# Optimization experiments

Measured on AMD Instinct MI355X. Metric: run time of the kernel, lower is better.

## Reference

```python
import jax, jax.numpy as jnp
import numpy as np
import jax.scipy.signal as jss

SX, SY, C, K = 256, 256, 3, 10
C0 = [0, 0, 0, 1, 1, 1, 2, 2, 2, 0]
C1 = [[0, 1, 2, 9], [3, 4, 5], [6, 7, 8]]
DD, DT, SIGMA = 5, 0.2, 0.65

_KX = jnp.array([[-1., 0., 1.], [-2., 0., 2.], [-1., 0., 1.]])
_KY = _KX.T


def _conv2(A, Kf):
    # zero-padded 'same' 2D true convolution, vmapped over channel axis
    return jax.vmap(lambda a: jss.convolve2d(a, Kf, mode='same'), in_axes=2, out_axes=2)(A)


def sobel(A):
    # (X, Y, c) -> (X, Y, 2, c): [sobel_y, sobel_x] stacked on axis 2 (FlowLenia convention)
    return jnp.concatenate([_conv2(A, _KY)[:, :, None, :], _conv2(A, _KX)[:, :, None, :]], axis=2)


def growth(U, m, s):
    # bell(U,m,s)*2 - 1
    return jnp.exp(-((U - m) / s) ** 2 / 2.) * 2. - 1.


def get_kernels_fft(R, r, a, w, b):
    # FlowLenia kernel construction: ring distance -> smooth cutoff * sum-of-bumps, normalized, fft2(fftshift)
    mid = SX // 2
    xs = jnp.arange(-mid, mid, dtype=jnp.float32)
    D = jnp.sqrt(xs[:, None] ** 2 + xs[None, :] ** 2)            # (X, Y)
    Dk = D[..., None] / ((R + 15.) * r)                          # (X, Y, k)
    ker = (b * jnp.exp(-(Dk[..., None] - a) ** 2 / w)).sum(-1)   # (X, Y, k)
    sig = 0.5 * (jnp.tanh(-(Dk - 1.) * 10. / 2.) + 1.)           # sigmoid(-(D-1)*10)
    Kk = sig * ker
    nK = Kk / Kk.sum(axis=(0, 1), keepdims=True)
    return jnp.fft.fft2(jnp.fft.fftshift(nK, axes=(0, 1)), axes=(0, 1))


def _rt_apply(A, F):
    # Reintegration tracking with 'wall' border: flow-driven mass redistribution over a (2dd+1)^2 neighborhood
    ii = jnp.arange(SX, dtype=jnp.float32)
    pos = jnp.stack(jnp.meshgrid(ii, ii, indexing='ij'), axis=-1) + 0.5   # (X, Y, 2) cell centers
    ma = DD - SIGMA                                   # max flow magnitude
    mu = pos[..., None] + jnp.clip(DT * F, -ma, ma)   # (X, Y, 2, C) target centers
    mu = jnp.clip(mu, SIGMA, SX - SIGMA)              # wall border
    offs = jnp.arange(-DD, DD + 1)
    gx, gy = jnp.meshgrid(offs, offs, indexing='ij')
    dxs, dys = gx.reshape(-1), gy.reshape(-1)
    clip_hi = min(1., 2. * SIGMA)

    def step(dx, dy):
        Ar = jnp.roll(A, (dx, dy), axis=(0, 1))
        mur = jnp.roll(mu, (dx, dy), axis=(0, 1))
        dpmu = jnp.abs(pos[..., None] - mur)                                  # (X, Y, 2, C)
        sz = 0.5 - dpmu + SIGMA
        area = jnp.prod(jnp.clip(sz, 0., clip_hi), axis=2) / (4. * SIGMA ** 2)  # (X, Y, C)
        return Ar * area

    return jax.vmap(step)(dxs, dys).sum(axis=0)


def setup_inputs() -> dict:
    key = jax.random.key(0)
    ks = jax.random.split(key, 9)
    A = jax.random.uniform(ks[0], (SX, SY, C), dtype=jnp.float32)
    R = jax.random.uniform(ks[1], (), minval=2.0, maxval=25.0)
    r = jax.random.uniform(ks[2], (K,), minval=0.2, maxval=1.0)
    m = jax.random.uniform(ks[3], (K,), minval=0.05, maxval=0.5)
    s = jax.random.uniform(ks[4], (K,), minval=0.001, maxval=0.18)
    h = jax.random.uniform(ks[5], (K,), minval=0.01, maxval=1.0)
    a = jax.random.uniform(ks[6], (K, 3), minval=0.0, maxval=1.0)
    b = jax.random.uniform(ks[7], (K, 3), minval=0.001, maxval=1.0)
    w = jax.random.uniform(ks[8], (K, 3), minval=0.01, maxval=0.5)
    return dict(A=A, R=R, r=r, m=m, s=s, h=h, a=a, b=b, w=w)


def reference(A, R, r, m, s, h, a, b, w):
    fK = get_kernels_fft(R, r, a, w, b)                       # (X, Y, k) complex
    fA = jnp.fft.fft2(A, axes=(0, 1))
    fAk = fA[:, :, jnp.array(C0)]                             # (X, Y, k)
    U = jnp.real(jnp.fft.ifft2(fK * fAk, axes=(0, 1)))        # (X, Y, k)
    U = growth(U, m, s) * h
    U = jnp.dstack([U[:, :, C1[c]].sum(axis=-1) for c in range(C)])  # (X, Y, C)
    nabla_U = sobel(U)                                        # (X, Y, 2, C)
    nabla_A = sobel(A.sum(axis=-1, keepdims=True))            # (X, Y, 2, 1)
    alpha = jnp.clip((A[:, :, None, :] / C) ** 2, 0., 1.)     # (X, Y, 1, C)
    F = nabla_U * (1. - alpha) - nabla_A * alpha              # (X, Y, 2, C)
    return _rt_apply(A, F)
```

## Files before the change

kernel.cpp:

```cpp
#include <hip/hip_runtime.h>

#define NPIX 65536

#define OX1ARE(c) ((0  + (c))*NPIX)
#define OX1AIM(c) ((3  + (c))*NPIX)
#define OX1K(k)   ((6  + (k))*NPIX)
#define OX2ARE(c) ((16 + (c))*NPIX)
#define OX2AIM(c) ((19 + (c))*NPIX)
#define OX2K(k)   ((22 + (k))*NPIX)
#define OX3RE(j)  ((32 + (j))*NPIX)
#define OX3IM(j)  ((37 + (j))*NPIX)
#define OU(k)     ((42 + (k))*NPIX)
#define OPACK(c)  ((52 + 4*(c))*NPIX)
#define OROWS     (64*NPIX)

__device__ __forceinline__ void fft256_core(float* __restrict__ re, float* __restrict__ im,
                                            const float* __restrict__ twr,
                                            const float* __restrict__ twi, int lane) {
    #pragma unroll
    for (int s = 1; s <= 8; ++s) {
        int h = 1 << (s - 1);
        #pragma unroll
        for (int b = 0; b < 2; ++b) {
            int idx = b*64 + lane;
            int pos = idx & (h - 1);
            int g   = idx >> (s - 1);
            int i0 = (g << s) + pos;
            int i1 = i0 + h;
            int tj = pos << (8 - s);
            float wr = twr[tj], wi = twi[tj];
            float xr = re[i1], xi = im[i1];
            float br = fmaf(xr, wr, -xi*wi);
            float bi = fmaf(xr, wi,  xi*wr);
            float ar = re[i0], ai = im[i0];
            re[i0] = ar + br; im[i0] = ai + bi;
            re[i1] = ar - br; im[i1] = ai - bi;
        }
    }
}

__device__ __forceinline__ void build_tw(float* twr, float* twi, int t, float sgn) {
    if (t < 128) {
        float ang = (float)t * 0.0245436930f;
        twr[t] = cosf(ang);
        twi[t] = sgn * sinf(ang);
    }
}

__device__ __forceinline__ void store_t4(float* __restrict__ dst, const float* __restrict__ buf,
                                         int off, int t, int lb) {
    float4 v;
    v.x = buf[0*512 + off + t];
    v.y = buf[1*512 + off + t];
    v.z = buf[2*512 + off + t];
    v.w = buf[3*512 + off + t];
    *(float4*)&dst[t*256 + lb] = v;
}

struct KP { float rden, a0,a1,a2, b0,b1,b2, iw0,iw1,iw2; };

__device__ __forceinline__ void load_kp(KP& kp, int k, float R,
        const float* __restrict__ r_, const float* __restrict__ a_,
        const float* __restrict__ b_, const float* __restrict__ w_) {
    kp.rden = 1.0f / ((R + 15.0f) * r_[k]);
    kp.a0 = a_[k*3+0]; kp.a1 = a_[k*3+1]; kp.a2 = a_[k*3+2];
    kp.b0 = b_[k*3+0]; kp.b1 = b_[k*3+1]; kp.b2 = b_[k*3+2];
    kp.iw0 = 1.0f/w_[k*3+0]; kp.iw1 = 1.0f/w_[k*3+1]; kp.iw2 = 1.0f/w_[k*3+2];
}

__device__ __forceinline__ float kval(int di, int dj, const KP& kp) {
    float D  = sqrtf((float)(di*di + dj*dj));
    float Dk = D * kp.rden;
    if (Dk > 3.0f) return 0.0f;
    float d0 = Dk - kp.a0, d1 = Dk - kp.a1, d2 = Dk - kp.a2;
    float ker = kp.b0*expf(-(d0*d0)*kp.iw0)
              + kp.b1*expf(-(d1*d1)*kp.iw1)
              + kp.b2*expf(-(d2*d2)*kp.iw2);
    float sig = 1.0f / (1.0f + expf(10.0f*(Dk - 1.0f)));
    return sig * ker;
}

__global__ __launch_bounds__(256) void fwd_rows(const float* __restrict__ A,
        const float* __restrict__ R_, const float* __restrict__ r_,
        const float* __restrict__ a_, const float* __restrict__ b_,
        const float* __restrict__ w_, float* __restrict__ ws) {
    __shared__ float buf[4*512];
    __shared__ float twr[128], twi[128];
    int p  = blockIdx.x >> 6;
    int lb = (blockIdx.x & 63) * 4;
    int wid = threadIdx.x >> 6, lane = threadIdx.x & 63;
    int t = threadIdx.x;
    build_tw(twr, twi, t, -1.0f);
    int iw = lb + wid;
    float* re = &buf[wid*512];
    float* im = re + 256;

    int fa, fb;
    switch (p) {
        case 0:  fa = 0;  fb = 1;  break;
        case 1:  fa = 2;  fb = 12; break;
        case 2:  fa = 3;  fb = 4;  break;
        case 3:  fa = 5;  fb = 6;  break;
        case 4:  fa = 7;  fb = 8;  break;
        case 5:  fa = 9;  fb = 10; break;
        default: fa = 11; fb = -1; break;
    }
    bool aA = (fa < 3);
    bool bA = (fb >= 0 && fb < 3);
    float R = R_[0];
    int di = ((iw + 128) & 255) - 128;
    KP kpa, kpb;
    if (!aA)      load_kp(kpa, fa - 3, R, r_, a_, b_, w_);
    if (fb >= 3)  load_kp(kpb, fb - 3, R, r_, a_, b_, w_);
    float sum_a = 0.0f, sum_b = 0.0f;
    #pragma unroll
    for (int e = 0; e < 4; ++e) {
        int idx = e*64 + lane;
        int dst = __brev(idx) >> 24;
        int dj  = ((idx + 128) & 255) - 128;
        float vf, vg;
        if (aA) vf = A[(iw*256 + idx)*3 + fa];
        else    { vf = kval(di, dj, kpa); sum_a += vf; }
        if (fb < 0)      vg = 0.0f;
        else if (bA)     vg = A[(iw*256 + idx)*3 + fb];
        else             { vg = kval(di, dj, kpb); sum_b += vg; }
        re[dst] = vf;
        im[dst] = vg;
    }
    if (!aA) {
        float s = sum_a;
        #pragma unroll
        for (int off = 32; off; off >>= 1) s += __shfl_xor(s, off);
        if (lane == 0) ws[OROWS + (fa - 3)*256 + iw] = s;
    }
    if (fb >= 3) {
        float s = sum_b;
        #pragma unroll
        for (int off = 32; off; off >>= 1) s += __shfl_xor(s, off);
        if (lane == 0) ws[OROWS + (fb - 3)*256 + iw] = s;
    }
    __syncthreads();
    fft256_core(re, im, twr, twi, lane);
    __syncthreads();
    if (t <= 128) {
        if (p <= 1) {
            int u2 = (256 - t) & 255;
            float4 Fre, Fim, Gre, Gim;
            float* pF[4] = {&Fre.x, &Fim.x, &Gre.x, &Gim.x};
            #pragma unroll
            for (int l = 0; l < 4; ++l) {
                float zr1 = buf[l*512 + t],  zi1 = buf[l*512 + 256 + t];
                float zr2 = buf[l*512 + u2], zi2 = buf[l*512 + 256 + u2];
                pF[0][l] = 0.5f*(zr1 + zr2);
                pF[1][l] = 0.5f*(zi1 - zi2);
                pF[2][l] = 0.5f*(zi1 + zi2);
                pF[3][l] = 0.5f*(zr2 - zr1);
            }
            if (p == 0) {
                *(float4*)&ws[OX1ARE(0) + t*256 + lb] = Fre;
                *(float4*)&ws[OX1AIM(0) + t*256 + lb] = Fim;
                *(float4*)&ws[OX1ARE(1) + t*256 + lb] = Gre;
                *(float4*)&ws[OX1AIM(1) + t*256 + lb] = Gim;
            } else {
                *(float4*)&ws[OX1ARE(2) + t*256 + lb] = Fre;
                *(float4*)&ws[OX1AIM(2) + t*256 + lb] = Fim;
                *(float4*)&ws[OX1K(9)   + t*256 + lb] = Gre;
            }
        } else {
            float4 va, vb;
            float* pV[2] = {&va.x, &vb.x};
            #pragma unroll
            for (int l = 0; l < 4; ++l) {
                pV[0][l] = buf[l*512 + t];
                pV[1][l] = buf[l*512 + 256 + t];
            }
            *(float4*)&ws[OX1K(fa - 3) + t*256 + lb] = va;
            if (fb >= 0) *(float4*)&ws[OX1K(fb - 3) + t*256 + lb] = vb;
        }
    }
}

__global__ __launch_bounds__(256) void fwd_cols(float* __restrict__ ws) {
    __shared__ float buf[4*512];
    __shared__ float twr[128], twi[128];
    int bid = blockIdx.x;
    int wid = threadIdx.x >> 6, lane = threadIdx.x & 63;
    int t = threadIdx.x;
    build_tw(twr, twi, t, -1.0f);
    float* re = &buf[wid*512];
    float* im = re + 256;
    if (bid < 99) {
        int c  = bid / 33;
        int ub = (bid % 33) * 4;
        int u  = ub + wid; if (u > 128) u = 128;
        const float* rr = ws + OX1ARE(c) + u*256;
        const float* ri = ws + OX1AIM(c) + u*256;
        #pragma unroll
        for (int e = 0; e < 4; ++e) {
            int idx = e*64 + lane;
            int dst = __brev(idx) >> 24;
            re[dst] = rr[idx];
            im[dst] = ri[idx];
        }
        __syncthreads();
        fft256_core(re, im, twr, twi, lane);
        __syncthreads();
        store_t4(ws + OX2ARE(c), buf, 0,   t, ub);
        store_t4(ws + OX2AIM(c), buf, 256, t, ub);
    } else {
        int q  = (bid - 99) / 33;
        int ub = ((bid - 99) % 33) * 4;
        int u  = ub + wid; if (u > 128) u = 128;
        const float* ra = ws + OX1K(2*q)     + u*256;
        const float* rb = ws + OX1K(2*q + 1) + u*256;
        #pragma unroll
        for (int e = 0; e < 4; ++e) {
            int idx = e*64 + lane;
            int dst = __brev(idx) >> 24;
            re[dst] = ra[idx];
            im[dst] = rb[idx];
        }
        __syncthreads();
        fft256_core(re, im, twr, twi, lane);
        __syncthreads();
        if (t <= 128) {
            store_t4(ws + OX2K(2*q),     buf, 0,   t, ub);
            store_t4(ws + OX2K(2*q + 1), buf, 256, t, ub);
        }
    }
}

__global__ __launch_bounds__(256) void inv_rows(float* __restrict__ ws) {
    __shared__ float buf[4*512];
    __shared__ float twr[128], twi[128];
    int j  = blockIdx.x >> 6;
    int lb = (blockIdx.x & 63) * 4;
    int wid = threadIdx.x >> 6, lane = threadIdx.x & 63;
    int t = threadIdx.x;
    build_tw(twr, twi, t, 1.0f);
    int ka = 2*j, kb = 2*j + 1;
    int ca = (ka < 9) ? ka/3 : 0;
    int cb = (kb < 9) ? kb/3 : 0;
    int v  = lb + wid;
    int vr = (256 - v) & 255;
    int vf = (v <= 128) ? v : 256 - v;
    const float* Aare_v = ws + OX2ARE(ca) + v*256;
    const float* Aaim_v = ws + OX2AIM(ca) + v*256;
    const float* Aare_r = ws + OX2ARE(ca) + vr*256;
    const float* Aaim_r = ws + OX2AIM(ca) + vr*256;
    const float* Bare_v = ws + OX2ARE(cb) + v*256;
    const float* Baim_v = ws + OX2AIM(cb) + v*256;
    const float* Bare_r = ws + OX2ARE(cb) + vr*256;
    const float* Baim_r = ws + OX2AIM(cb) + vr*256;
    const float* Ka = ws + OX2K(ka) + vf*256;
    const float* Kb = ws + OX2K(kb) + vf*256;
    float* re = &buf[wid*512];
    float* im = re + 256;
    #pragma unroll
    for (int e = 0; e < 4; ++e) {
        int idx = e*64 + lane;
        int dst = __brev(idx) >> 24;
        bool hi = idx > 128;
        int uf = hi ? 256 - idx : idx;
        const float* pAr = hi ? Aare_r : Aare_v;
        const float* pAi = hi ? Aaim_r : Aaim_v;
        const float* pBr = hi ? Bare_r : Bare_v;
        const float* pBi = hi ? Baim_r : Baim_v;
        float ar = pAr[uf];
        float ai = pAi[uf]; ai = hi ? -ai : ai;
        float br = pBr[uf];
        float bi = pBi[uf]; bi = hi ? -bi : bi;
        float kva = Ka[uf], kvb = Kb[uf];
        float uar = ar*kva, uai = ai*kva;
        float ubr = br*kvb, ubi = bi*kvb;
        re[dst] = uar - ubi;
        im[dst] = uai + ubr;
    }
    __syncthreads();
    fft256_core(re, im, twr, twi, lane);
    __syncthreads();
    store_t4(ws + OX3RE(j), buf, 0,   t, lb);
    store_t4(ws + OX3IM(j), buf, 256, t, lb);
}

__global__ __launch_bounds__(256) void inv_cols(float* __restrict__ ws) {
    __shared__ float buf[4*512];
    __shared__ float twr[128], twi[128];
    int j  = blockIdx.x >> 6;
    int lb = (blockIdx.x & 63) * 4;
    int wid = threadIdx.x >> 6, lane = threadIdx.x & 63;
    int t = threadIdx.x;
    build_tw(twr, twi, t, 1.0f);
    float* re = &buf[wid*512];
    float* im = re + 256;
    const float* rr = ws + OX3RE(j) + (lb + wid)*256;
    const float* ri = ws + OX3IM(j) + (lb + wid)*256;
    #pragma unroll
    for (int e = 0; e < 4; ++e) {
        int idx = e*64 + lane;
        int dst = __brev(idx) >> 24;
        re[dst] = rr[idx];
        im[dst] = ri[idx];
    }
    __syncthreads();
    fft256_core(re, im, twr, twi, lane);
    __syncthreads();
    const float sc = 1.0f / 65536.0f;
    float4 va, vb;
    va.x = buf[0*512 + t] * sc;       vb.x = buf[0*512 + 256 + t] * sc;
    va.y = buf[1*512 + t] * sc;       vb.y = buf[1*512 + 256 + t] * sc;
    va.z = buf[2*512 + t] * sc;       vb.z = buf[2*512 + 256 + t] * sc;
    va.w = buf[3*512 + t] * sc;       vb.w = buf[3*512 + 256 + t] * sc;
    *(float4*)&ws[OU(2*j)     + t*256 + lb] = va;
    *(float4*)&ws[OU(2*j + 1) + t*256 + lb] = vb;
}

__global__ __launch_bounds__(256) void growth_mu(const float* __restrict__ A,
                                                 float* __restrict__ ws,
                                                 const float* __restrict__ m_,
                                                 const float* __restrict__ s_,
                                                 const float* __restrict__ h_) {
    __shared__ float Ush[3][256];
    __shared__ float As[3][256];
    __shared__ float kinv[4];
    int b = blockIdx.x;
    int c = b >> 8;
    int x = b & 255;
    int t = threadIdx.x, wid = t >> 6, lane = t & 63;
    int nk = (c == 0) ? 4 : 3;
    if (wid < nk) {
        int k = (wid == 3) ? 9 : c*3 + wid;
        const float* rw = ws + OROWS + k*256;
        float v = rw[lane] + rw[64+lane] + rw[128+lane] + rw[192+lane];
        #pragma unroll
        for (int off = 32; off; off >>= 1) v += __shfl_xor(v, off);
        if (lane == 0) kinv[wid] = 1.0f / v;
    }
    #pragma unroll
    for (int rr = 0; rr < 3; ++rr) {
        int xr = x - 1 + rr;
        float sv = 0.0f;
        if (xr >= 0 && xr <= 255) {
            int base = (xr*256 + t)*3;
            sv = A[base] + A[base + 1] + A[base + 2];
        }
        As[rr][t] = sv;
    }
    __syncthreads();
    for (int rr = 0; rr < 3; ++rr) {
        int xr = x - 1 + rr;
        float outv = 0.0f;
        if (xr >= 0 && xr <= 255) {
            int idx = xr*256 + t;
            for (int kk = 0; kk < nk; ++kk) {
                int k = (kk == 3) ? 9 : c*3 + kk;
                float U = ws[OU(k) + idx] * kinv[kk];
                float z = (U - m_[k]) / s_[k];
                outv += h_[k] * (expf(-0.5f*z*z)*2.0f - 1.0f);
            }
        }
        Ush[rr][t] = outv;
    }
    __syncthreads();
    int y = t;
    float vA[3][3], vU[3][3];
    #pragma unroll
    for (int ii = 0; ii < 3; ++ii)
        #pragma unroll
        for (int jj = 0; jj < 3; ++jj) {
            int yy = y - 1 + jj;
            bool ok = (yy >= 0 && yy <= 255);
            vA[ii][jj] = ok ? As[ii][yy]  : 0.0f;
            vU[ii][jj] = ok ? Ush[ii][yy] : 0.0f;
        }
    float gyA = (vA[0][0] + 2.0f*vA[0][1] + vA[0][2]) - (vA[2][0] + 2.0f*vA[2][1] + vA[2][2]);
    float gxA = (vA[0][0] + 2.0f*vA[1][0] + vA[2][0]) - (vA[0][2] + 2.0f*vA[1][2] + vA[2][2]);
    float gy  = (vU[0][0] + 2.0f*vU[0][1] + vU[0][2]) - (vU[2][0] + 2.0f*vU[2][1] + vU[2][2]);
    float gx  = (vU[0][0] + 2.0f*vU[1][0] + vU[2][0]) - (vU[0][2] + 2.0f*vU[1][2] + vU[2][2]);
    float a = A[(x*256 + y)*3 + c];
    float al = (a / 3.0f); al = al * al;
    al = fminf(fmaxf(al, 0.0f), 1.0f);
    float F0 = gy * (1.0f - al) - gyA * al;
    float F1 = gx * (1.0f - al) - gxA * al;
    float d0 = fminf(fmaxf(0.2f * F0, -4.35f), 4.35f);
    float d1 = fminf(fmaxf(0.2f * F1, -4.35f), 4.35f);
    float mux = fminf(fmaxf((float)x + 0.5f + d0, 0.65f), 255.35f);
    float muy = fminf(fmaxf((float)y + 0.5f + d1, 0.65f), 255.35f);
    float4 pk;
    pk.x = a;
    pk.y = mux - ((float)x + 0.5f);
    pk.z = muy;
    pk.w = 0.0f;
    *(float4*)&ws[OPACK(c) + (x*256 + y)*4] = pk;
}

__global__ __launch_bounds__(256) void rt_apply_v3(const float* __restrict__ ws,
                                                   float* __restrict__ out) {
    __shared__ float4 sP[11*256];
    int b = blockIdx.x;
    int c = b >> 8;
    int x = b & 255;
    const float4* pp = (const float4*)&ws[OPACK(c)];
    int t = threadIdx.x;
    #pragma unroll
    for (int i = 0; i < 11; ++i) {
        int xs = (x - (i - 5)) & 255;
        sP[i*256 + t] = pp[xs*256 + t];
    }
    __syncthreads();
    int y = t;
    float py = (float)y + 0.5f;
    float acc = 0.0f;
    #pragma unroll
    for (int i = 0; i < 11; ++i) {
        int xs = (x - (i - 5)) & 255;
        float dxf = (float)(x - xs);
        int rb = i * 256;
        #pragma unroll
        for (int dy = -5; dy <= 5; ++dy) {
            int sy = (y - dy) & 255;
            float4 v = sP[rb + sy];
            float ax = __builtin_amdgcn_fmed3f(1.15f - fabsf(dxf - v.y), 0.0f, 1.0f);
            float ay = __builtin_amdgcn_fmed3f(1.15f - fabsf(py  - v.z), 0.0f, 1.0f);
            acc = fmaf(v.x, ax * ay, acc);
        }
    }
    out[(x*256 + y)*3 + c] = acc * (1.0f / (4.0f * 0.65f * 0.65f));
}

extern "C" void kernel_launch(void* const* d_in, const int* in_sizes, int n_in,
                              void* d_out, int out_size, void* d_ws, size_t ws_size,
                              hipStream_t stream) {
    const float* A = (const float*)d_in[0];
    const float* R = (const float*)d_in[1];
    const float* r = (const float*)d_in[2];
    const float* m = (const float*)d_in[3];
    const float* s = (const float*)d_in[4];
    const float* h = (const float*)d_in[5];
    const float* a = (const float*)d_in[6];
    const float* b = (const float*)d_in[7];
    const float* w = (const float*)d_in[8];
    float* ws  = (float*)d_ws;
    float* out = (float*)d_out;

    fwd_rows<<<7*64, 256, 0, stream>>>(A, R, r, a, b, w, ws);
    fwd_cols<<<99 + 165, 256, 0, stream>>>(ws);
    inv_rows<<<5*64, 256, 0, stream>>>(ws);
    inv_cols<<<5*64, 256, 0, stream>>>(ws);
    growth_mu<<<768, 256, 0, stream>>>(A, ws, m, s, h);
    rt_apply_v3<<<768, 256, 0, stream>>>(ws, out);
}
```

Measured before the change: 112.1 us.

## Scatter reintegration with atomics and fold growth into inverse FFT

Replaces the gather-based reintegration kernel, which evaluated 121 neighbours per output cell, with a scatter formulation. Each source cell computes its at most 3x3 nonzero bilinear footprint and adds it to the output with atomicAdd, and the output is zeroed inside inv_cols. Kernel normalization moves into the kernel-spectrum columns pass and the growth function into the inverse-column FFT epilogue, which removes one launch and the packed intermediate buffer. The cost is atomic contention and a summation order that is no longer deterministic.

```diff
diff --git a/kernel.cpp b/kernel.cpp
--- a/kernel.cpp
+++ b/kernel.cpp
@@ -11,8 +11,7 @@
 #define OX3RE(j)  ((32 + (j))*NPIX)
 #define OX3IM(j)  ((37 + (j))*NPIX)
 #define OU(k)     ((42 + (k))*NPIX)
-#define OPACK(c)  ((52 + 4*(c))*NPIX)
-#define OROWS     (64*NPIX)
+#define OROWS     (52*NPIX)
 
 __device__ __forceinline__ void fft256_core(float* __restrict__ re, float* __restrict__ im,
                                             const float* __restrict__ twr,
@@ -183,6 +182,7 @@
 __global__ __launch_bounds__(256) void fwd_cols(float* __restrict__ ws) {
     __shared__ float buf[4*512];
     __shared__ float twr[128], twi[128];
+    __shared__ float kks[2];
     int bid = blockIdx.x;
     int wid = threadIdx.x >> 6, lane = threadIdx.x & 63;
     int t = threadIdx.x;
@@ -211,6 +211,13 @@
         int q  = (bid - 99) / 33;
         int ub = ((bid - 99) % 33) * 4;
         int u  = ub + wid; if (u > 128) u = 128;
+        if (wid < 2) {
+            const float* rw = ws + OROWS + (2*q + wid)*256;
+            float v = rw[lane] + rw[64+lane] + rw[128+lane] + rw[192+lane];
+            #pragma unroll
+            for (int off = 32; off; off >>= 1) v += __shfl_xor(v, off);
+            if (lane == 0) kks[wid] = 1.0f / (v * 65536.0f);
+        }
         const float* ra = ws + OX1K(2*q)     + u*256;
         const float* rb = ws + OX1K(2*q + 1) + u*256;
         #pragma unroll
@@ -224,8 +231,14 @@
         fft256_core(re, im, twr, twi, lane);
         __syncthreads();
         if (t <= 128) {
-            store_t4(ws + OX2K(2*q),     buf, 0,   t, ub);
-            store_t4(ws + OX2K(2*q + 1), buf, 256, t, ub);
+            float sa = kks[0], sb = kks[1];
+            float4 va, vb;
+            va.x = buf[0*512 + t]*sa;  vb.x = buf[0*512 + 256 + t]*sb;
+            va.y = buf[1*512 + t]*sa;  vb.y = buf[1*512 + 256 + t]*sb;
+            va.z = buf[2*512 + t]*sa;  vb.z = buf[2*512 + 256 + t]*sb;
+            va.w = buf[3*512 + t]*sa;  vb.w = buf[3*512 + 256 + t]*sb;
+            *(float4*)&ws[OX2K(2*q)     + t*256 + ub] = va;
+            *(float4*)&ws[OX2K(2*q + 1) + t*256 + ub] = vb;
         }
     }
 }
@@ -283,7 +296,11 @@
     store_t4(ws + OX3IM(j), buf, 256, t, lb);
 }
 
-__global__ __launch_bounds__(256) void inv_cols(float* __restrict__ ws) {
+__global__ __launch_bounds__(256) void inv_cols(float* __restrict__ ws,
+                                                const float* __restrict__ m_,
+                                                const float* __restrict__ s_,
+                                                const float* __restrict__ h_,
+                                                float* __restrict__ out) {
     __shared__ float buf[4*512];
     __shared__ float twr[128], twi[128];
     int j  = blockIdx.x >> 6;
@@ -291,6 +308,10 @@
     int wid = threadIdx.x >> 6, lane = threadIdx.x & 63;
     int t = threadIdx.x;
     build_tw(twr, twi, t, 1.0f);
+    {
+        int gid = blockIdx.x * 256 + t;
+        if (gid < 49152) ((float4*)out)[gid] = make_float4(0.f, 0.f, 0.f, 0.f);
+    }
     float* re = &buf[wid*512];
     float* im = re + 256;
     const float* rr = ws + OX3RE(j) + (lb + wid)*256;
@@ -305,61 +326,47 @@
     __syncthreads();
     fft256_core(re, im, twr, twi, lane);
     __syncthreads();
-    const float sc = 1.0f / 65536.0f;
+    int k0 = 2*j, k1 = 2*j + 1;
+    float m0 = m_[k0], m1 = m_[k1];
+    float c0 = 0.5f/(s_[k0]*s_[k0]), c1 = 0.5f/(s_[k1]*s_[k1]);
+    float h0 = h_[k0], h1 = h_[k1];
     float4 va, vb;
-    va.x = buf[0*512 + t] * sc;       vb.x = buf[0*512 + 256 + t] * sc;
-    va.y = buf[1*512 + t] * sc;       vb.y = buf[1*512 + 256 + t] * sc;
-    va.z = buf[2*512 + t] * sc;       vb.z = buf[2*512 + 256 + t] * sc;
-    va.w = buf[3*512 + t] * sc;       vb.w = buf[3*512 + 256 + t] * sc;
-    *(float4*)&ws[OU(2*j)     + t*256 + lb] = va;
-    *(float4*)&ws[OU(2*j + 1) + t*256 + lb] = vb;
-}
-
-__global__ __launch_bounds__(256) void growth_mu(const float* __restrict__ A,
-                                                 float* __restrict__ ws,
-                                                 const float* __restrict__ m_,
-                                                 const float* __restrict__ s_,
-                                                 const float* __restrict__ h_) {
-    __shared__ float Ush[3][256];
+    #pragma unroll
+    for (int l = 0; l < 4; ++l) {
+        float u0 = buf[l*512 + t]       - m0;
+        float u1 = buf[l*512 + 256 + t] - m1;
+        (&va.x)[l] = h0 * fmaf(2.0f, expf(-(u0*u0)*c0), -1.0f);
+        (&vb.x)[l] = h1 * fmaf(2.0f, expf(-(u1*u1)*c1), -1.0f);
+    }
+    *(float4*)&ws[OU(k0) + t*256 + lb] = va;
+    *(float4*)&ws[OU(k1) + t*256 + lb] = vb;
+}
+
+__global__ __launch_bounds__(256) void growth_scatter(const float* __restrict__ A,
+                                                      const float* __restrict__ ws,
+                                                      float* __restrict__ out) {
+    __shared__ float Gs[3][256];
     __shared__ float As[3][256];
-    __shared__ float kinv[4];
     int b = blockIdx.x;
     int c = b >> 8;
     int x = b & 255;
-    int t = threadIdx.x, wid = t >> 6, lane = t & 63;
+    int t = threadIdx.x;
     int nk = (c == 0) ? 4 : 3;
-    if (wid < nk) {
-        int k = (wid == 3) ? 9 : c*3 + wid;
-        const float* rw = ws + OROWS + k*256;
-        float v = rw[lane] + rw[64+lane] + rw[128+lane] + rw[192+lane];
-        #pragma unroll
-        for (int off = 32; off; off >>= 1) v += __shfl_xor(v, off);
-        if (lane == 0) kinv[wid] = 1.0f / v;
-    }
     #pragma unroll
     for (int rr = 0; rr < 3; ++rr) {
         int xr = x - 1 + rr;
-        float sv = 0.0f;
-        if (xr >= 0 && xr <= 255) {
-            int base = (xr*256 + t)*3;
-            sv = A[base] + A[base + 1] + A[base + 2];
-        }
-        As[rr][t] = sv;
-    }
-    __syncthreads();
-    for (int rr = 0; rr < 3; ++rr) {
-        int xr = x - 1 + rr;
-        float outv = 0.0f;
+        float sv = 0.0f, gv = 0.0f;
         if (xr >= 0 && xr <= 255) {
             int idx = xr*256 + t;
+            int base = idx*3;
+            sv = A[base] + A[base + 1] + A[base + 2];
             for (int kk = 0; kk < nk; ++kk) {
                 int k = (kk == 3) ? 9 : c*3 + kk;
-                float U = ws[OU(k) + idx] * kinv[kk];
-                float z = (U - m_[k]) / s_[k];
-                outv += h_[k] * (expf(-0.5f*z*z)*2.0f - 1.0f);
+                gv += ws[OU(k) + idx];
             }
         }
-        Ush[rr][t] = outv;
+        As[rr][t] = sv;
+        Gs[rr][t] = gv;
     }
     __syncthreads();
     int y = t;
@@ -370,8 +377,8 @@
         for (int jj = 0; jj < 3; ++jj) {
             int yy = y - 1 + jj;
             bool ok = (yy >= 0 && yy <= 255);
-            vA[ii][jj] = ok ? As[ii][yy]  : 0.0f;
-            vU[ii][jj] = ok ? Ush[ii][yy] : 0.0f;
+            vA[ii][jj] = ok ? As[ii][yy] : 0.0f;
+            vU[ii][jj] = ok ? Gs[ii][yy] : 0.0f;
         }
     float gyA = (vA[0][0] + 2.0f*vA[0][1] + vA[0][2]) - (vA[2][0] + 2.0f*vA[2][1] + vA[2][2]);
     float gxA = (vA[0][0] + 2.0f*vA[1][0] + vA[2][0]) - (vA[0][2] + 2.0f*vA[1][2] + vA[2][2]);
@@ -386,46 +393,31 @@
     float d1 = fminf(fmaxf(0.2f * F1, -4.35f), 4.35f);
     float mux = fminf(fmaxf((float)x + 0.5f + d0, 0.65f), 255.35f);
     float muy = fminf(fmaxf((float)y + 0.5f + d1, 0.65f), 255.35f);
-    float4 pk;
-    pk.x = a;
-    pk.y = mux - ((float)x + 0.5f);
-    pk.z = muy;
-    pk.w = 0.0f;
-    *(float4*)&ws[OPACK(c) + (x*256 + y)*4] = pk;
-}
-
-__global__ __launch_bounds__(256) void rt_apply_v3(const float* __restrict__ ws,
-                                                   float* __restrict__ out) {
-    __shared__ float4 sP[11*256];
-    int b = blockIdx.x;
-    int c = b >> 8;
-    int x = b & 255;
-    const float4* pp = (const float4*)&ws[OPACK(c)];
-    int t = threadIdx.x;
-    #pragma unroll
-    for (int i = 0; i < 11; ++i) {
-        int xs = (x - (i - 5)) & 255;
-        sP[i*256 + t] = pp[xs*256 + t];
-    }
-    __syncthreads();
-    int y = t;
-    float py = (float)y + 0.5f;
-    float acc = 0.0f;
-    #pragma unroll
-    for (int i = 0; i < 11; ++i) {
-        int xs = (x - (i - 5)) & 255;
-        float dxf = (float)(x - xs);
-        int rb = i * 256;
-        #pragma unroll
-        for (int dy = -5; dy <= 5; ++dy) {
-            int sy = (y - dy) & 255;
-            float4 v = sP[rb + sy];
-            float ax = __builtin_amdgcn_fmed3f(1.15f - fabsf(dxf - v.y), 0.0f, 1.0f);
-            float ay = __builtin_amdgcn_fmed3f(1.15f - fabsf(py  - v.z), 0.0f, 1.0f);
-            acc = fmaf(v.x, ax * ay, acc);
-        }
-    }
-    out[(x*256 + y)*3 + c] = acc * (1.0f / (4.0f * 0.65f * 0.65f));
+    float dxp = mux - ((float)x + 0.5f);
+    float dyp = muy - ((float)y + 0.5f);
+    int bx = (int)ceilf(dxp - 1.15f);
+    int by = (int)ceilf(dyp - 1.15f);
+    float wx[3], wy[3];
+    #pragma unroll
+    for (int q = 0; q < 3; ++q) {
+        wx[q] = __builtin_amdgcn_fmed3f(1.15f - fabsf((float)(bx + q) - dxp), 0.0f, 1.0f);
+        wy[q] = __builtin_amdgcn_fmed3f(1.15f - fabsf((float)(by + q) - dyp), 0.0f, 1.0f);
+    }
+    float am = a * (1.0f / (4.0f * 0.65f * 0.65f));
+    #pragma unroll
+    for (int qx = 0; qx < 3; ++qx) {
+        float wxa = am * wx[qx];
+        if (wxa == 0.0f) continue;
+        int xd = (x + bx + qx) & 255;
+        #pragma unroll
+        for (int qy = 0; qy < 3; ++qy) {
+            float wgt = wxa * wy[qy];
+            if (wgt != 0.0f) {
+                int yd = (y + by + qy) & 255;
+                atomicAdd(&out[(xd*256 + yd)*3 + c], wgt);
+            }
+        }
+    }
 }
 
 extern "C" void kernel_launch(void* const* d_in, const int* in_sizes, int n_in,
@@ -446,7 +438,6 @@
     fwd_rows<<<7*64, 256, 0, stream>>>(A, R, r, a, b, w, ws);
     fwd_cols<<<99 + 165, 256, 0, stream>>>(ws);
     inv_rows<<<5*64, 256, 0, stream>>>(ws);
-    inv_cols<<<5*64, 256, 0, stream>>>(ws);
-    growth_mu<<<768, 256, 0, stream>>>(A, ws, m, s, h);
-    rt_apply_v3<<<768, 256, 0, stream>>>(ws, out);
-}
+    inv_cols<<<5*64, 256, 0, stream>>>(ws, m, s, h, out);
+    growth_scatter<<<768, 256, 0, stream>>>(A, ws, out);
+}
```

Result: slower. 117.3 us (+4.6%).
